# Kernel tuning notes

Hardware: AMD Instinct MI355X
Metric: run time of the kernel (lower is better)

The kernel has to match this reference:

```python
import jax, jax.numpy as jnp
import numpy as np

R = 1.1
SCALE = 100.0
BUMP_STEPS = 32
NUM_THETAS = 32
NUM_FEATURES = 128
N_NODES = 200000
NUM_GRAPHS = 128


def setup_inputs() -> dict:
    key = jax.random.key(0)
    k1, k2, k3 = jax.random.split(key, 3)
    x = jax.random.normal(k1, (N_NODES, NUM_FEATURES), dtype=jnp.float32)
    batch = jnp.sort(jax.random.randint(k2, (N_NODES,), 0, NUM_GRAPHS, dtype=jnp.int64))
    v = jax.random.uniform(k3, (NUM_THETAS, NUM_FEATURES), dtype=jnp.float32) - 0.5
    return {"x": x, "batch": batch, "num_graphs": NUM_GRAPHS, "v": v}


def reference(x, batch, num_graphs, v):
    # nh: node heights along each direction theta -> [N, T]
    nh = x @ v.T
    # linspace over filtration values -> [S]
    lin = jnp.linspace(-R, R, BUMP_STEPS, dtype=nh.dtype)
    # bump: sigmoid difference; second point is the constant pad value R
    # ecc: [N, S, T]  (node-major so segment_sum reduces the leading axis)
    ecc = (jax.nn.sigmoid(SCALE * (lin[None, :, None] - nh[:, None, :]))
           - jax.nn.sigmoid(SCALE * (lin - R))[None, :, None])
    # scatter-add per graph label -> [ng, S, T] == index_add over dim1 then movedim(0,1)
    ect = jax.ops.segment_sum(ecc, batch, num_segments=num_graphs)
    return ect
```

## Files before the change

kernel.cpp:

```cpp
#include <hip/hip_runtime.h>
#include <math.h>

#define N_NODES 200000
#define NF 128
#define NT 32
#define NS 32
#define NG 128
#define ATILE 256
#define NTILES 8
#define VSTRIDE 136
#define HPAD 33

typedef short bf16x8 __attribute__((ext_vector_type(8)));
typedef float floatx4 __attribute__((ext_vector_type(4)));

__device__ __forceinline__ float rcp_fast(float x) { return __builtin_amdgcn_rcpf(x); }

__device__ __forceinline__ void split_bf16(float f, unsigned short& h, unsigned short& l) {
    unsigned u  = __float_as_uint(f);
    unsigned r  = u + 0x7FFFu + ((u >> 16) & 1u);
    unsigned hb = r & 0xFFFF0000u;
    h = (unsigned short)(hb >> 16);
    float rem = f - __uint_as_float(hb);
    unsigned u2 = __float_as_uint(rem);
    unsigned r2 = u2 + 0x7FFFu + ((u2 >> 16) & 1u);
    l = (unsigned short)(r2 >> 16);
}

__device__ __forceinline__ void split8(float4 a, float4 b, bf16x8& h8, bf16x8& l8) {
    unsigned short h[8], l[8];
    split_bf16(a.x, h[0], l[0]); split_bf16(a.y, h[1], l[1]);
    split_bf16(a.z, h[2], l[2]); split_bf16(a.w, h[3], l[3]);
    split_bf16(b.x, h[4], l[4]); split_bf16(b.y, h[5], l[5]);
    split_bf16(b.z, h[6], l[6]); split_bf16(b.w, h[7], l[7]);
    h8 = (bf16x8){(short)h[0],(short)h[1],(short)h[2],(short)h[3],
                  (short)h[4],(short)h[5],(short)h[6],(short)h[7]};
    l8 = (bf16x8){(short)l[0],(short)l[1],(short)l[2],(short)l[3],
                  (short)l[4],(short)l[5],(short)l[6],(short)l[7]};
}

__device__ __forceinline__ void deposit(float* corr, int b, float z, float Lw, float C1) {
    float s0f = ceilf(z - 1.0f);
    int   s0  = (int)s0f;
    float e0  = __builtin_amdgcn_exp2f(Lw * (z - s0f));
    float e1  = e0 * C1;
    float f0  = rcp_fast(1.0f + e0);
    float f1  = rcp_fast(1.0f + e1);
    atomicAdd(&corr[b + max(s0, 0)], f0);
    int sB = s0 + 1; if (sB < 32) atomicAdd(&corr[b + sB], f1 - f0);
    int sC = s0 + 2; if (sC < 32) atomicAdd(&corr[b + sC], 1.0f - f1);
}

__global__ __launch_bounds__(256)
void graph_starts(const int* __restrict__ batch, int* __restrict__ starts) {
    int i = blockIdx.x * 256 + threadIdx.x;
    if (i >= N_NODES) return;
    int b    = batch[i];
    int prev = (i == 0) ? -1 : batch[i - 1];
    for (int g = prev + 1; g <= b; ++g) starts[g] = i;
    if (i == N_NODES - 1)
        for (int g = b + 1; g <= NG; ++g) starts[g] = N_NODES;
}

__global__ __launch_bounds__(256, 7)
void ect_tile(const float* __restrict__ x,
              const float* __restrict__ v,
              const int* __restrict__ starts,
              float* __restrict__ partials,
              float* __restrict__ out,
              int use_ws)
{
    __shared__ __align__(16) unsigned short vh[NT * VSTRIDE];
    __shared__ __align__(16) unsigned short vl[NT * VSTRIDE];
    __shared__ float corr[NT * HPAD];

    const int tid  = threadIdx.x;
    const int t    = blockIdx.x;
    const int g    = blockIdx.y;
    const int w    = tid >> 6;
    const int lane = tid & 63;
    const int mrow = lane & 15;
    const int quad = lane >> 4;

    const int start = starts[g];
    const int count = starts[g + 1] - start;
    const int slot  = g * NTILES + t;

    if (t * ATILE >= count) {
        if (use_ws) {
            float4 z4 = {0.f, 0.f, 0.f, 0.f};
            *(float4*)&partials[(size_t)slot * 1024 + tid * 4] = z4;
        }
        return;
    }
    const int base   = start + t * ATILE;
    const int nvalid = min(ATILE, count - t * ATILE);
    const int nsub   = (nvalid + 63) >> 6;

    #pragma unroll
    for (int j = 0; j < 4; ++j) {
        int idx4 = j * 256 + tid;
        int row  = idx4 >> 5;
        int f4   = idx4 & 31;
        float4 val = *(const float4*)&v[(size_t)row * NF + f4 * 4];
        unsigned short h0,h1,h2,h3,l0,l1,l2,l3;
        split_bf16(val.x, h0, l0); split_bf16(val.y, h1, l1);
        split_bf16(val.z, h2, l2); split_bf16(val.w, h3, l3);
        uint2 hh, ll;
        hh.x = (unsigned)h0 | ((unsigned)h1 << 16); hh.y = (unsigned)h2 | ((unsigned)h3 << 16);
        ll.x = (unsigned)l0 | ((unsigned)l1 << 16); ll.y = (unsigned)l2 | ((unsigned)l3 << 16);
        *(uint2*)&vh[row * VSTRIDE + f4 * 4] = hh;
        *(uint2*)&vl[row * VSTRIDE + f4 * 4] = ll;
    }
    for (int i = tid; i < NT * HPAD; i += 256) corr[i] = 0.0f;
    __syncthreads();

    const float inv_dlin = 14.090909090909092f;
    const float Lw       = 10.23848093f;
    const float dlin     = 2.2f / 31.0f;
    const float L        = 144.26950408889634f;
    const float C1       = 8.2777115e-04f;

    const int b0base = mrow * VSTRIDE + quad * 8;
    const int b1base = (16 + mrow) * VSTRIDE + quad * 8;
    const int c0base = mrow * HPAD;
    const int c1base = (16 + mrow) * HPAD;

    float c0 = 0.f, c1 = 0.f;

    for (int k = 0; k < nsub; ++k) {
        const int gi = min(base + k * 64 + w * 16 + mrow, N_NODES - 1);
        const float* __restrict__ xrow = x + (size_t)gi * NF + quad * 8;
        bf16x8 ah[4], al[4];
        #pragma unroll
        for (int slice = 0; slice < 4; ++slice) {
            float4 a0 = *(const float4*)&xrow[slice * 32];
            float4 a1 = *(const float4*)&xrow[slice * 32 + 4];
            split8(a0, a1, ah[slice], al[slice]);
        }

        floatx4 acc0 = {0.f, 0.f, 0.f, 0.f};
        floatx4 acc1 = {0.f, 0.f, 0.f, 0.f};
        #pragma unroll
        for (int slice = 0; slice < 4; ++slice) {
            bf16x8 bh0 = *(bf16x8*)&vh[b0base + slice * 32];
            bf16x8 bl0 = *(bf16x8*)&vl[b0base + slice * 32];
            bf16x8 bh1 = *(bf16x8*)&vh[b1base + slice * 32];
            bf16x8 bl1 = *(bf16x8*)&vl[b1base + slice * 32];
            acc0 = __builtin_amdgcn_mfma_f32_16x16x32_bf16(ah[slice], bh0, acc0, 0, 0, 0);
            acc0 = __builtin_amdgcn_mfma_f32_16x16x32_bf16(ah[slice], bl0, acc0, 0, 0, 0);
            acc0 = __builtin_amdgcn_mfma_f32_16x16x32_bf16(al[slice], bh0, acc0, 0, 0, 0);
            acc1 = __builtin_amdgcn_mfma_f32_16x16x32_bf16(ah[slice], bh1, acc1, 0, 0, 0);
            acc1 = __builtin_amdgcn_mfma_f32_16x16x32_bf16(ah[slice], bl1, acc1, 0, 0, 0);
            acc1 = __builtin_amdgcn_mfma_f32_16x16x32_bf16(al[slice], bh1, acc1, 0, 0, 0);
        }

        const int nloc = k * 64 + w * 16 + quad * 4;
        #pragma unroll
        for (int reg = 0; reg < 4; ++reg) {
            if (nloc + reg < nvalid) {
                {
                    float z = fmaf(acc0[reg], inv_dlin, 15.5f);
                    if (z <= -1.0f)      c0 += 1.0f;
                    else if (z < 32.0f)  deposit(corr, c0base, z, Lw, C1);
                }
                {
                    float z = fmaf(acc1[reg], inv_dlin, 15.5f);
                    if (z <= -1.0f)      c1 += 1.0f;
                    else if (z < 32.0f)  deposit(corr, c1base, z, Lw, C1);
                }
            }
        }
    }
    if (c0 != 0.f) atomicAdd(&corr[c0base], c0);
    if (c1 != 0.f) atomicAdd(&corr[c1base], c1);
    __syncthreads();

    {
        const int grp = tid >> 5;
        const int sc  = tid & 31;
        for (int row = grp; row < NT; row += 8) {
            float val = corr[row * HPAD + sc];
            #pragma unroll
            for (int d = 1; d < 32; d <<= 1) {
                float nbr = __shfl_up(val, d, 32);
                if (sc >= d) val += nbr;
            }
            corr[row * HPAD + sc] = val;
        }
    }
    __syncthreads();

    const float cnt  = (float)nvalid;
    const int   s    = tid >> 3;
    const int   ft0  = (tid & 7) * 4;
    const float lin_s = -1.1f + (float)s * dlin;
    const float cs    = rcp_fast(1.0f + __builtin_amdgcn_exp2f(L * (1.1f - lin_s)));
    float4 r;
    r.x = corr[(ft0 + 0) * HPAD + s] - cnt * cs;
    r.y = corr[(ft0 + 1) * HPAD + s] - cnt * cs;
    r.z = corr[(ft0 + 2) * HPAD + s] - cnt * cs;
    r.w = corr[(ft0 + 3) * HPAD + s] - cnt * cs;
    if (use_ws) {
        *(float4*)&partials[(size_t)slot * 1024 + tid * 4] = r;
    } else {
        float* o = out + (size_t)g * (NS * NT) + tid * 4;
        atomicAdd(&o[0], r.x); atomicAdd(&o[1], r.y);
        atomicAdd(&o[2], r.z); atomicAdd(&o[3], r.w);
    }
}

__global__ __launch_bounds__(256)
void reduce_partials(const float* __restrict__ partials, float* __restrict__ out) {
    const int g   = blockIdx.x;
    const int tid = threadIdx.x;
    const float4* p4 = (const float4*)partials;
    float4 acc = {0.f, 0.f, 0.f, 0.f};
    #pragma unroll
    for (int t = 0; t < NTILES; ++t) {
        float4 v = p4[(size_t)(g * NTILES + t) * 256 + tid];
        acc.x += v.x; acc.y += v.y; acc.z += v.z; acc.w += v.w;
    }
    ((float4*)out)[(size_t)g * 256 + tid] = acc;
}

extern "C" void kernel_launch(void* const* d_in, const int* in_sizes, int n_in,
                              void* d_out, int out_size, void* d_ws, size_t ws_size,
                              hipStream_t stream) {
    const float* x     = (const float*)d_in[0];
    const int*   batch = (const int*)d_in[1];
    const float* v     = (const float*)d_in[3];
    float*       out   = (float*)d_out;

    int*   starts   = (int*)d_ws;
    float* partials = (float*)((char*)d_ws + 1024);
    const size_t need = 1024 + (size_t)NG * NTILES * 1024 * sizeof(float);
    const int use_ws  = (ws_size >= need) ? 1 : 0;

    hipMemsetAsync(d_out, 0, (size_t)out_size * sizeof(float), stream);
    graph_starts<<<dim3((N_NODES + 255) / 256), dim3(256), 0, stream>>>(batch, starts);
    ect_tile<<<dim3(NTILES, NG), dim3(256), 0, stream>>>(x, v, starts, partials, out, use_ws);
    if (use_ws)
        reduce_partials<<<dim3(NG), dim3(256), 0, stream>>>(partials, out);
}
```

Measured before the change: 210.9 us.

## Shrink per-block node tile to 64 and precompute bf16-split directions once

Each block now handles one 64-node subtile instead of looping over four. This gives roughly four times more blocks per graph, so global-load latency is hidden by parallelism rather than a serial loop. The x-row loads are issued before the shared-memory staging of v so they overlap. A small new prep kernel splits v into bf16 hi/lo once, and the main kernel copies those halves from the workspace instead of recomputing the split in every block. The cost is more partial buffers: 30 per graph instead of 8, which adds write and reduce traffic and per-block setup such as zeroing, the scan and v staging. Graphs larger than 1920 nodes would no longer be covered.

```diff
diff --git a/kernel.cpp b/kernel.cpp
--- a/kernel.cpp
+++ b/kernel.cpp
@@ -1,4 +1,5 @@
 #include <hip/hip_runtime.h>
+#include <hip/hip_bf16.h>
 #include <math.h>
 
 #define N_NODES 200000
@@ -6,8 +7,8 @@
 #define NT 32
 #define NS 32
 #define NG 128
-#define ATILE 256
-#define NTILES 8
+#define ATILE 64
+#define NTILES 30
 #define VSTRIDE 136
 #define HPAD 33
 
@@ -16,23 +17,24 @@
 
 __device__ __forceinline__ float rcp_fast(float x) { return __builtin_amdgcn_rcpf(x); }
 
-__device__ __forceinline__ void split_bf16(float f, unsigned short& h, unsigned short& l) {
-    unsigned u  = __float_as_uint(f);
-    unsigned r  = u + 0x7FFFu + ((u >> 16) & 1u);
-    unsigned hb = r & 0xFFFF0000u;
-    h = (unsigned short)(hb >> 16);
-    float rem = f - __uint_as_float(hb);
-    unsigned u2 = __float_as_uint(rem);
-    unsigned r2 = u2 + 0x7FFFu + ((u2 >> 16) & 1u);
-    l = (unsigned short)(r2 >> 16);
+__device__ __forceinline__ unsigned short bf16_bits(float f) {
+    __hip_bfloat16 h = __float2bfloat16(f);
+    unsigned short u; __builtin_memcpy(&u, &h, 2); return u;
+}
+__device__ __forceinline__ float bf16_val(unsigned short u) {
+    unsigned v = (unsigned)u << 16; float f; __builtin_memcpy(&f, &v, 4); return f;
+}
+__device__ __forceinline__ void split1(float f, unsigned short& h, unsigned short& l) {
+    h = bf16_bits(f);
+    l = bf16_bits(f - bf16_val(h));
 }
 
 __device__ __forceinline__ void split8(float4 a, float4 b, bf16x8& h8, bf16x8& l8) {
     unsigned short h[8], l[8];
-    split_bf16(a.x, h[0], l[0]); split_bf16(a.y, h[1], l[1]);
-    split_bf16(a.z, h[2], l[2]); split_bf16(a.w, h[3], l[3]);
-    split_bf16(b.x, h[4], l[4]); split_bf16(b.y, h[5], l[5]);
-    split_bf16(b.z, h[6], l[6]); split_bf16(b.w, h[7], l[7]);
+    split1(a.x, h[0], l[0]); split1(a.y, h[1], l[1]);
+    split1(a.z, h[2], l[2]); split1(a.w, h[3], l[3]);
+    split1(b.x, h[4], l[4]); split1(b.y, h[5], l[5]);
+    split1(b.z, h[6], l[6]); split1(b.w, h[7], l[7]);
     h8 = (bf16x8){(short)h[0],(short)h[1],(short)h[2],(short)h[3],
                   (short)h[4],(short)h[5],(short)h[6],(short)h[7]};
     l8 = (bf16x8){(short)l[0],(short)l[1],(short)l[2],(short)l[3],
@@ -62,10 +64,33 @@
         for (int g = b + 1; g <= NG; ++g) starts[g] = N_NODES;
 }
 
-__global__ __launch_bounds__(256, 7)
+__global__ __launch_bounds__(256)
+void vprep(const float* __restrict__ v,
+           unsigned short* __restrict__ vth,
+           unsigned short* __restrict__ vtl)
+{
+    const int tid = threadIdx.x;
+    #pragma unroll
+    for (int j = 0; j < 4; ++j) {
+        int idx4 = tid * 4 + j;
+        float4 val = ((const float4*)v)[idx4];
+        unsigned short h0,h1,h2,h3,l0,l1,l2,l3;
+        split1(val.x, h0, l0); split1(val.y, h1, l1);
+        split1(val.z, h2, l2); split1(val.w, h3, l3);
+        uint2 hh, ll;
+        hh.x = (unsigned)h0 | ((unsigned)h1 << 16); hh.y = (unsigned)h2 | ((unsigned)h3 << 16);
+        ll.x = (unsigned)l0 | ((unsigned)l1 << 16); ll.y = (unsigned)l2 | ((unsigned)l3 << 16);
+        *(uint2*)&vth[idx4 * 4] = hh;
+        *(uint2*)&vtl[idx4 * 4] = ll;
+    }
+}
+
+__global__ __launch_bounds__(256, 6)
 void ect_tile(const float* __restrict__ x,
               const float* __restrict__ v,
               const int* __restrict__ starts,
+              const unsigned short* __restrict__ vth,
+              const unsigned short* __restrict__ vtl,
               float* __restrict__ partials,
               float* __restrict__ out,
               int use_ws)
@@ -95,25 +120,68 @@
     }
     const int base   = start + t * ATILE;
     const int nvalid = min(ATILE, count - t * ATILE);
-    const int nsub   = (nvalid + 63) >> 6;
-
-    #pragma unroll
-    for (int j = 0; j < 4; ++j) {
-        int idx4 = j * 256 + tid;
-        int row  = idx4 >> 5;
-        int f4   = idx4 & 31;
-        float4 val = *(const float4*)&v[(size_t)row * NF + f4 * 4];
-        unsigned short h0,h1,h2,h3,l0,l1,l2,l3;
-        split_bf16(val.x, h0, l0); split_bf16(val.y, h1, l1);
-        split_bf16(val.z, h2, l2); split_bf16(val.w, h3, l3);
-        uint2 hh, ll;
-        hh.x = (unsigned)h0 | ((unsigned)h1 << 16); hh.y = (unsigned)h2 | ((unsigned)h3 << 16);
-        ll.x = (unsigned)l0 | ((unsigned)l1 << 16); ll.y = (unsigned)l2 | ((unsigned)l3 << 16);
-        *(uint2*)&vh[row * VSTRIDE + f4 * 4] = hh;
-        *(uint2*)&vl[row * VSTRIDE + f4 * 4] = ll;
+
+    const int gi = min(base + w * 16 + mrow, N_NODES - 1);
+    const float* __restrict__ xrow = x + (size_t)gi * NF + quad * 8;
+    float4 xa[8];
+    #pragma unroll
+    for (int slice = 0; slice < 4; ++slice) {
+        xa[2 * slice]     = *(const float4*)&xrow[slice * 32];
+        xa[2 * slice + 1] = *(const float4*)&xrow[slice * 32 + 4];
+    }
+
+    if (use_ws) {
+        #pragma unroll
+        for (int j = 0; j < 4; ++j) {
+            int idx4 = j * 256 + tid;
+            int row  = idx4 >> 5;
+            int f4   = idx4 & 31;
+            *(uint2*)&vh[row * VSTRIDE + f4 * 4] = *(const uint2*)&vth[idx4 * 4];
+            *(uint2*)&vl[row * VSTRIDE + f4 * 4] = *(const uint2*)&vtl[idx4 * 4];
+        }
+    } else {
+        #pragma unroll
+        for (int j = 0; j < 4; ++j) {
+            int idx4 = j * 256 + tid;
+            int row  = idx4 >> 5;
+            int f4   = idx4 & 31;
+            float4 val = *(const float4*)&v[(size_t)row * NF + f4 * 4];
+            unsigned short h0,h1,h2,h3,l0,l1,l2,l3;
+            split1(val.x, h0, l0); split1(val.y, h1, l1);
+            split1(val.z, h2, l2); split1(val.w, h3, l3);
+            uint2 hh, ll;
+            hh.x = (unsigned)h0 | ((unsigned)h1 << 16); hh.y = (unsigned)h2 | ((unsigned)h3 << 16);
+            ll.x = (unsigned)l0 | ((unsigned)l1 << 16); ll.y = (unsigned)l2 | ((unsigned)l3 << 16);
+            *(uint2*)&vh[row * VSTRIDE + f4 * 4] = hh;
+            *(uint2*)&vl[row * VSTRIDE + f4 * 4] = ll;
+        }
     }
     for (int i = tid; i < NT * HPAD; i += 256) corr[i] = 0.0f;
+
+    bf16x8 ah[4], al[4];
+    #pragma unroll
+    for (int slice = 0; slice < 4; ++slice)
+        split8(xa[2 * slice], xa[2 * slice + 1], ah[slice], al[slice]);
     __syncthreads();
+
+    const int b0base = mrow * VSTRIDE + quad * 8;
+    const int b1base = (16 + mrow) * VSTRIDE + quad * 8;
+
+    floatx4 acc0 = {0.f, 0.f, 0.f, 0.f};
+    floatx4 acc1 = {0.f, 0.f, 0.f, 0.f};
+    #pragma unroll
+    for (int slice = 0; slice < 4; ++slice) {
+        bf16x8 bh0 = *(bf16x8*)&vh[b0base + slice * 32];
+        bf16x8 bl0 = *(bf16x8*)&vl[b0base + slice * 32];
+        bf16x8 bh1 = *(bf16x8*)&vh[b1base + slice * 32];
+        bf16x8 bl1 = *(bf16x8*)&vl[b1base + slice * 32];
+        acc0 = __builtin_amdgcn_mfma_f32_16x16x32_bf16(ah[slice], bh0, acc0, 0, 0, 0);
+        acc0 = __builtin_amdgcn_mfma_f32_16x16x32_bf16(ah[slice], bl0, acc0, 0, 0, 0);
+        acc0 = __builtin_amdgcn_mfma_f32_16x16x32_bf16(al[slice], bh0, acc0, 0, 0, 0);
+        acc1 = __builtin_amdgcn_mfma_f32_16x16x32_bf16(ah[slice], bh1, acc1, 0, 0, 0);
+        acc1 = __builtin_amdgcn_mfma_f32_16x16x32_bf16(ah[slice], bl1, acc1, 0, 0, 0);
+        acc1 = __builtin_amdgcn_mfma_f32_16x16x32_bf16(al[slice], bh1, acc1, 0, 0, 0);
+    }
 
     const float inv_dlin = 14.090909090909092f;
     const float Lw       = 10.23848093f;
@@ -121,54 +189,23 @@
     const float L        = 144.26950408889634f;
     const float C1       = 8.2777115e-04f;
 
-    const int b0base = mrow * VSTRIDE + quad * 8;
-    const int b1base = (16 + mrow) * VSTRIDE + quad * 8;
     const int c0base = mrow * HPAD;
     const int c1base = (16 + mrow) * HPAD;
 
     float c0 = 0.f, c1 = 0.f;
-
-    for (int k = 0; k < nsub; ++k) {
-        const int gi = min(base + k * 64 + w * 16 + mrow, N_NODES - 1);
-        const float* __restrict__ xrow = x + (size_t)gi * NF + quad * 8;
-        bf16x8 ah[4], al[4];
-        #pragma unroll
-        for (int slice = 0; slice < 4; ++slice) {
-            float4 a0 = *(const float4*)&xrow[slice * 32];
-            float4 a1 = *(const float4*)&xrow[slice * 32 + 4];
-            split8(a0, a1, ah[slice], al[slice]);
-        }
-
-        floatx4 acc0 = {0.f, 0.f, 0.f, 0.f};
-        floatx4 acc1 = {0.f, 0.f, 0.f, 0.f};
-        #pragma unroll
-        for (int slice = 0; slice < 4; ++slice) {
-            bf16x8 bh0 = *(bf16x8*)&vh[b0base + slice * 32];
-            bf16x8 bl0 = *(bf16x8*)&vl[b0base + slice * 32];
-            bf16x8 bh1 = *(bf16x8*)&vh[b1base + slice * 32];
-            bf16x8 bl1 = *(bf16x8*)&vl[b1base + slice * 32];
-            acc0 = __builtin_amdgcn_mfma_f32_16x16x32_bf16(ah[slice], bh0, acc0, 0, 0, 0);
-            acc0 = __builtin_amdgcn_mfma_f32_16x16x32_bf16(ah[slice], bl0, acc0, 0, 0, 0);
-            acc0 = __builtin_amdgcn_mfma_f32_16x16x32_bf16(al[slice], bh0, acc0, 0, 0, 0);
-            acc1 = __builtin_amdgcn_mfma_f32_16x16x32_bf16(ah[slice], bh1, acc1, 0, 0, 0);
-            acc1 = __builtin_amdgcn_mfma_f32_16x16x32_bf16(ah[slice], bl1, acc1, 0, 0, 0);
-            acc1 = __builtin_amdgcn_mfma_f32_16x16x32_bf16(al[slice], bh1, acc1, 0, 0, 0);
-        }
-
-        const int nloc = k * 64 + w * 16 + quad * 4;
-        #pragma unroll
-        for (int reg = 0; reg < 4; ++reg) {
-            if (nloc + reg < nvalid) {
-                {
-                    float z = fmaf(acc0[reg], inv_dlin, 15.5f);
-                    if (z <= -1.0f)      c0 += 1.0f;
-                    else if (z < 32.0f)  deposit(corr, c0base, z, Lw, C1);
-                }
-                {
-                    float z = fmaf(acc1[reg], inv_dlin, 15.5f);
-                    if (z <= -1.0f)      c1 += 1.0f;
-                    else if (z < 32.0f)  deposit(corr, c1base, z, Lw, C1);
-                }
+    const int nloc = w * 16 + quad * 4;
+    #pragma unroll
+    for (int reg = 0; reg < 4; ++reg) {
+        if (nloc + reg < nvalid) {
+            {
+                float z = fmaf(acc0[reg], inv_dlin, 15.5f);
+                if (z <= -1.0f)      c0 += 1.0f;
+                else if (z < 32.0f)  deposit(corr, c0base, z, Lw, C1);
+            }
+            {
+                float z = fmaf(acc1[reg], inv_dlin, 15.5f);
+                if (z <= -1.0f)      c1 += 1.0f;
+                else if (z < 32.0f)  deposit(corr, c1base, z, Lw, C1);
             }
         }
     }
@@ -232,14 +269,19 @@
     const float* v     = (const float*)d_in[3];
     float*       out   = (float*)d_out;
 
-    int*   starts   = (int*)d_ws;
-    float* partials = (float*)((char*)d_ws + 1024);
-    const size_t need = 1024 + (size_t)NG * NTILES * 1024 * sizeof(float);
+    int*            starts   = (int*)d_ws;
+    unsigned short* vth      = (unsigned short*)((char*)d_ws + 1024);
+    unsigned short* vtl      = (unsigned short*)((char*)d_ws + 1024 + 8192);
+    float*          partials = (float*)((char*)d_ws + 1024 + 16384);
+    const size_t need = 1024 + 16384 + (size_t)NG * NTILES * 1024 * sizeof(float);
     const int use_ws  = (ws_size >= need) ? 1 : 0;
 
     hipMemsetAsync(d_out, 0, (size_t)out_size * sizeof(float), stream);
     graph_starts<<<dim3((N_NODES + 255) / 256), dim3(256), 0, stream>>>(batch, starts);
-    ect_tile<<<dim3(NTILES, NG), dim3(256), 0, stream>>>(x, v, starts, partials, out, use_ws);
+    if (use_ws)
+        vprep<<<dim3(1), dim3(256), 0, stream>>>(v, vth, vtl);
+    ect_tile<<<dim3(NTILES, NG), dim3(256), 0, stream>>>(x, v, starts, vth, vtl,
+                                                         partials, out, use_ws);
     if (use_ws)
         reduce_partials<<<dim3(NG), dim3(256), 0, stream>>>(partials, out);
 }
```

New measurement: 173.6 us. -17.7%, faster.
